# Kernel tuning notes

Measured on AMD Instinct MI355X. Metric: run time of the kernel, lower is better.

The kernel has to match this reference:

```python
import jax, jax.numpy as jnp
import numpy as np

N_HEADS = 16


def setup_inputs() -> dict:
    key = jax.random.key(0)
    k1, k2, k3 = jax.random.split(key, 3)
    B, T, D = 2, 2048, 1024
    x = jax.random.normal(k1, (B, T, D), dtype=jnp.float32)
    w_qkv = jax.random.normal(k2, (3 * D, D), dtype=jnp.float32) * 0.02
    w_proj = jax.random.normal(k3, (D, D), dtype=jnp.float32) * (0.02 / np.sqrt(24.0))
    return {"x": x, "w_qkv": w_qkv, "w_proj": w_proj}


def reference(x, w_qkv, w_proj):
    B, T, D = x.shape
    H = N_HEADS
    dh = D // H
    # qkv linear (no bias): x @ w_qkv.T -> [B, T, 3D]
    qkv = jnp.einsum('btd,ed->bte', x, w_qkv)
    q, k, v = jnp.split(qkv, 3, axis=-1)
    q = q.reshape(B, T, H, dh)
    k = k.reshape(B, T, H, dh)
    v = v.reshape(B, T, H, dh)
    # attention with materialized scores [B, H, T, S]
    scores = jnp.einsum('bthd,bshd->bhts', q, k) / jnp.sqrt(jnp.asarray(dh, x.dtype))
    attn = jax.nn.softmax(scores.astype(jnp.float32), axis=-1).astype(x.dtype)
    out = jnp.einsum('bhts,bshd->bthd', attn, v).reshape(B, T, D)
    # output projection (no bias)
    return jnp.einsum('btd,ed->bte', out, w_proj)
```

## Files before the change

### kernel.cpp

```cpp
#include <hip/hip_runtime.h>


typedef __attribute__((ext_vector_type(8))) short s8v;
typedef __attribute__((ext_vector_type(8))) unsigned short us8;
typedef __attribute__((ext_vector_type(4))) unsigned short us4;
typedef __attribute__((ext_vector_type(4))) float f4v;
typedef __attribute__((ext_vector_type(16))) float f16v;
typedef __attribute__((ext_vector_type(4))) unsigned u4v;

__device__ __forceinline__ unsigned short f2b(float f) {
    unsigned u = __builtin_bit_cast(unsigned, f);
    u += 0x7FFFu + ((u >> 16) & 1u);
    return (unsigned short)(u >> 16);
}
__device__ __forceinline__ unsigned packtrunc(float a, float b, unsigned sel) {
    unsigned r;
    asm("v_perm_b32 %0, %1, %2, %3"
        : "=v"(r)
        : "v"(__builtin_bit_cast(unsigned, b)), "v"(__builtin_bit_cast(unsigned, a)), "s"(sel));
    return r;
}

#if __has_builtin(__builtin_amdgcn_exp2f)
#define EXP2F(x) __builtin_amdgcn_exp2f(x)
#else
#define EXP2F(x) exp2f(x)
#endif

#define QSCALE 0.18033688011112042f

__global__ __launch_bounds__(256) void cvt_all(const float* __restrict__ x,
                                               const float* __restrict__ wq,
                                               const float* __restrict__ wp,
                                               unsigned short* __restrict__ xb,
                                               unsigned short* __restrict__ wqb,
                                               unsigned short* __restrict__ wpb) {
    const int nx = 4096 * 1024 / 4, nq = 3072 * 1024 / 4;
    int i = blockIdx.x * 256 + threadIdx.x;
    const float* s;
    unsigned short* d;
    int j;
    if (i < nx)           { s = x;  d = xb;  j = i; }
    else if (i < nx + nq) { s = wq; d = wqb; j = i - nx; }
    else                  { s = wp; d = wpb; j = i - nx - nq; }
    float4 v = ((const float4*)s)[j];
    ushort4 o;
    o.x = f2b(v.x); o.y = f2b(v.y); o.z = f2b(v.z); o.w = f2b(v.w);
    ((ushort4*)d)[j] = o;
}

#define GLD_LDS16(g, l)                                                                        \
    __builtin_amdgcn_global_load_lds((const __attribute__((address_space(1))) unsigned*)(g),   \
                                     (__attribute__((address_space(3))) unsigned*)(l), 16, 0, 0)

__global__ __launch_bounds__(256) void gemm_qkv(const unsigned short* __restrict__ A,
                                                const unsigned short* __restrict__ B,
                                                unsigned short* __restrict__ qkvb) {
    __shared__ unsigned short As[128][64];
    __shared__ unsigned short Bs[128][64];
    const int tid = threadIdx.x;
    const int l = tid & 63, w = tid >> 6;
    const int quad = l >> 4, ln = l & 15;
    const int m0 = blockIdx.y * 128, n0 = blockIdx.x * 128;
    const int wm = (w >> 1) * 64, wn = (w & 1) * 64;

    const f4v fz = {0.f, 0.f, 0.f, 0.f};
    f4v acc[4][4];
#pragma unroll
    for (int i = 0; i < 4; ++i)
#pragma unroll
        for (int j = 0; j < 4; ++j) acc[i][j] = fz;

    const int srow = tid >> 3, sc8 = tid & 7;
    const int gcol = ((sc8 ^ (srow & 7)) << 3);
    const int koff0 = ((quad ^ (ln & 7)) << 3);
    const int koff1 = (((4 + quad) ^ (ln & 7)) << 3);

    for (int k0 = 0; k0 < 1024; k0 += 64) {
#pragma unroll
        for (int b = 0; b < 4; ++b) {
            GLD_LDS16(A + (size_t)(m0 + srow + 32 * b) * 1024 + k0 + gcol, &As[srow + 32 * b][sc8 * 8]);
            GLD_LDS16(B + (size_t)(n0 + srow + 32 * b) * 1024 + k0 + gcol, &Bs[srow + 32 * b][sc8 * 8]);
        }
        __syncthreads();
#pragma unroll
        for (int ks = 0; ks < 2; ++ks) {
            const int ko = ks ? koff1 : koff0;
            s8v af[4], bf[4];
#pragma unroll
            for (int mt = 0; mt < 4; ++mt) af[mt] = *(const s8v*)&As[wm + mt * 16 + ln][ko];
#pragma unroll
            for (int nt = 0; nt < 4; ++nt) bf[nt] = *(const s8v*)&Bs[wn + nt * 16 + ln][ko];
#pragma unroll
            for (int mt = 0; mt < 4; ++mt)
#pragma unroll
                for (int nt = 0; nt < 4; ++nt)
                    acc[mt][nt] = __builtin_amdgcn_mfma_f32_16x16x32_bf16(af[mt], bf[nt], acc[mt][nt], 0, 0, 0);
        }
        __syncthreads();
    }

#pragma unroll
    for (int mt = 0; mt < 4; ++mt)
#pragma unroll
        for (int nt = 0; nt < 4; ++nt) {
            const int col = n0 + wn + nt * 16 + ln;
            const int row = m0 + wm + mt * 16 + quad * 4;
            const float sc = (col < 1024) ? QSCALE : 1.0f;
#pragma unroll
            for (int r = 0; r < 4; ++r)
                qkvb[(size_t)(row + r) * 3072 + col] = f2b(acc[mt][nt][r] * sc);
        }
}

__global__ __launch_bounds__(256) void gemm_proj(const unsigned short* __restrict__ A,
                                                 const unsigned short* __restrict__ B,
                                                 float* __restrict__ C) {
    __shared__ unsigned short As[128][64];
    __shared__ unsigned short Bs[64][64];
    const int tid = threadIdx.x;
    const int l = tid & 63, w = tid >> 6;
    const int quad = l >> 4, ln = l & 15;
    const int m0 = blockIdx.y * 128, n0 = blockIdx.x * 64;
    const int wm = w * 32;

    const f4v fz = {0.f, 0.f, 0.f, 0.f};
    f4v acc[2][4];
#pragma unroll
    for (int i = 0; i < 2; ++i)
#pragma unroll
        for (int j = 0; j < 4; ++j) acc[i][j] = fz;

    const int srow = tid >> 3, sc8 = tid & 7;
    const int gcol = ((sc8 ^ (srow & 7)) << 3);
    const int koff0 = ((quad ^ (ln & 7)) << 3);
    const int koff1 = (((4 + quad) ^ (ln & 7)) << 3);

    for (int k0 = 0; k0 < 1024; k0 += 64) {
#pragma unroll
        for (int b = 0; b < 4; ++b)
            GLD_LDS16(A + (size_t)(m0 + srow + 32 * b) * 1024 + k0 + gcol, &As[srow + 32 * b][sc8 * 8]);
#pragma unroll
        for (int b = 0; b < 2; ++b)
            GLD_LDS16(B + (size_t)(n0 + srow + 32 * b) * 1024 + k0 + gcol, &Bs[srow + 32 * b][sc8 * 8]);
        __syncthreads();
#pragma unroll
        for (int ks = 0; ks < 2; ++ks) {
            const int ko = ks ? koff1 : koff0;
            s8v af[2], bf[4];
#pragma unroll
            for (int mt = 0; mt < 2; ++mt) af[mt] = *(const s8v*)&As[wm + mt * 16 + ln][ko];
#pragma unroll
            for (int nt = 0; nt < 4; ++nt) bf[nt] = *(const s8v*)&Bs[nt * 16 + ln][ko];
#pragma unroll
            for (int mt = 0; mt < 2; ++mt)
#pragma unroll
                for (int nt = 0; nt < 4; ++nt)
                    acc[mt][nt] = __builtin_amdgcn_mfma_f32_16x16x32_bf16(af[mt], bf[nt], acc[mt][nt], 0, 0, 0);
        }
        __syncthreads();
    }

#pragma unroll
    for (int mt = 0; mt < 2; ++mt)
#pragma unroll
        for (int nt = 0; nt < 4; ++nt) {
            const int row = m0 + wm + mt * 16 + quad * 4;
            const int col = n0 + nt * 16 + ln;
#pragma unroll
            for (int r = 0; r < 4; ++r) C[(size_t)(row + r) * 1024 + col] = acc[mt][nt][r];
        }
}

__global__ __launch_bounds__(256, 4) void attn_split(const unsigned short* __restrict__ qkvb,
                                                     float* __restrict__ opart,
                                                     float* __restrict__ lpart) {
    __shared__ unsigned short Ks[2][64][76];
    __shared__ unsigned short Vt[2][64][76];

    const int tid = threadIdx.x;
    const int l = tid & 63, w = tid >> 6;
    const int m31 = l & 31, h2 = l >> 5;
    const int qw = w * 32;
    const int t0 = blockIdx.x * 128;
    const int hh = blockIdx.y;
    const int bb = blockIdx.z >> 1, sp = blockIdx.z & 1;
    const size_t rowbase = (size_t)bb * 2048;
    const int sbase = sp * 1024;
    const unsigned sel = 0x07060302u;

#pragma unroll
    for (int it = 0; it < 4; ++it) {
        const int idx = tid + it * 256;
        const int qr = idx >> 3, qc = (idx & 7) * 8;
        unsigned short* dst = (qr < 64) ? &Ks[0][qr][qc] : &Ks[1][qr - 64][qc];
        *(us8*)dst = *(const us8*)(qkvb + (rowbase + t0 + qr) * 3072 + hh * 64 + qc);
    }
    __syncthreads();
    s8v qf[4];
    {
        const int qrow = qw + m31;
#pragma unroll
        for (int k4 = 0; k4 < 4; ++k4)
            qf[k4] = (qrow < 64) ? *(const s8v*)&Ks[0][qrow][k4 * 16 + h2 * 8]
                                 : *(const s8v*)&Ks[1][qrow - 64][k4 * 16 + h2 * 8];
    }
    __syncthreads();

    const int r0 = tid >> 3, c0 = (tid & 7) * 8;
    const int va = tid >> 4, vc = tid & 15;

    f16v zz;
#pragma unroll
    for (int i = 0; i < 16; ++i) zz[i] = 0.f;
    f16v oacc[2];
    oacc[0] = zz; oacc[1] = zz;
    float lsum = 0.f;

    us8 kreg0 = *(const us8*)(qkvb + (rowbase + sbase + r0) * 3072 + 1024 + hh * 64 + c0);
    us8 kreg1 = *(const us8*)(qkvb + (rowbase + sbase + r0 + 32) * 3072 + 1024 + hh * 64 + c0);
    us4 vreg[4];
#pragma unroll
    for (int j = 0; j < 4; ++j)
        vreg[j] = *(const us4*)(qkvb + (rowbase + sbase + 4 * va + j) * 3072 + 2048 + hh * 64 + 4 * vc);
    *(us8*)&Ks[0][r0][c0] = kreg0;
    *(us8*)&Ks[0][r0 + 32][c0] = kreg1;
#pragma unroll
    for (int dd = 0; dd < 4; ++dd) {
        unsigned lo = (unsigned)vreg[0][dd] | ((unsigned)vreg[1][dd] << 16);
        unsigned hi = (unsigned)vreg[2][dd] | ((unsigned)vreg[3][dd] << 16);
        uint2 pk2; pk2.x = lo; pk2.y = hi;
        *(uint2*)&Vt[0][4 * vc + dd][4 * va] = pk2;
    }

    for (int i = 0; i < 16; ++i) {
        const int cur = i & 1;
        __syncthreads();

        if (i + 1 < 16) {
            const size_t sn = rowbase + sbase + (i + 1) * 64;
            kreg0 = *(const us8*)(qkvb + (sn + r0) * 3072 + 1024 + hh * 64 + c0);
            kreg1 = *(const us8*)(qkvb + (sn + r0 + 32) * 3072 + 1024 + hh * 64 + c0);
#pragma unroll
            for (int j = 0; j < 4; ++j)
                vreg[j] = *(const us4*)(qkvb + (sn + 4 * va + j) * 3072 + 2048 + hh * 64 + 4 * vc);
        }

#pragma unroll
        for (int st = 0; st < 2; ++st) {
            f16v sacc = zz;
            __builtin_amdgcn_s_setprio(1);
#pragma unroll
            for (int k4 = 0; k4 < 4; ++k4) {
                s8v kf = *(const s8v*)&Ks[cur][st * 32 + m31][k4 * 16 + h2 * 8];
                sacc = __builtin_amdgcn_mfma_f32_32x32x16_bf16(kf, qf[k4], sacc, 0, 0, 0);
            }
            __builtin_amdgcn_s_setprio(0);
            unsigned wv[4][2];
#pragma unroll
            for (int g = 0; g < 4; ++g) {
                float p0 = EXP2F(sacc[g * 4 + 0]);
                float p1 = EXP2F(sacc[g * 4 + 1]);
                float p2 = EXP2F(sacc[g * 4 + 2]);
                float p3 = EXP2F(sacc[g * 4 + 3]);
                lsum += (p0 + p1) + (p2 + p3);
                wv[g][0] = packtrunc(p0, p1, sel);
                wv[g][1] = packtrunc(p2, p3, sel);
            }
            __builtin_amdgcn_s_setprio(1);
#pragma unroll
            for (int e = 0; e < 2; ++e) {
                auto ra = __builtin_amdgcn_permlane32_swap(wv[2 * e][0], wv[2 * e + 1][0], false, false);
                auto rb = __builtin_amdgcn_permlane32_swap(wv[2 * e][1], wv[2 * e + 1][1], false, false);
                u4v t;
                t[0] = ra[0]; t[1] = rb[0];
                t[2] = ra[1]; t[3] = rb[1];
                s8v pf = __builtin_bit_cast(s8v, t);
                const int k2 = 2 * st + e;
#pragma unroll
                for (int nt = 0; nt < 2; ++nt) {
                    s8v vfr = *(const s8v*)&Vt[cur][nt * 32 + m31][k2 * 16 + h2 * 8];
                    oacc[nt] = __builtin_amdgcn_mfma_f32_32x32x16_bf16(pf, vfr, oacc[nt], 0, 0, 0);
                }
            }
            __builtin_amdgcn_s_setprio(0);
        }

        if (i + 1 < 16) {
            *(us8*)&Ks[1 - cur][r0][c0] = kreg0;
            *(us8*)&Ks[1 - cur][r0 + 32][c0] = kreg1;
#pragma unroll
            for (int dd = 0; dd < 4; ++dd) {
                unsigned lo = (unsigned)vreg[0][dd] | ((unsigned)vreg[1][dd] << 16);
                unsigned hi = (unsigned)vreg[2][dd] | ((unsigned)vreg[3][dd] << 16);
                uint2 pk2; pk2.x = lo; pk2.y = hi;
                *(uint2*)&Vt[1 - cur][4 * vc + dd][4 * va] = pk2;
            }
        }
    }

    lsum += __shfl_xor(lsum, 32, 64);
    if (h2 == 0)
        lpart[((size_t)sp * 4096 + rowbase + t0 + qw + m31) * 16 + hh] = lsum;

    float* op = opart + (size_t)sp * 4096 * 1024;
#pragma unroll
    for (int nt = 0; nt < 2; ++nt)
#pragma unroll
        for (int g = 0; g < 4; ++g)
#pragma unroll
            for (int r = 0; r < 4; ++r) {
                const int qrow = 8 * g + 4 * h2 + r;
                op[(rowbase + t0 + qw + qrow) * 1024 + hh * 64 + nt * 32 + m31] = oacc[nt][g * 4 + r];
            }
}

__global__ __launch_bounds__(256) void attn_combine(const float* __restrict__ opart,
                                                    const float* __restrict__ lpart,
                                                    unsigned short* __restrict__ attnb) {
    const int idx = blockIdx.x * 256 + threadIdx.x;
    const int r = idx >> 8, c4 = (idx & 255) << 2, h = c4 >> 6;
    const size_t fi = (size_t)r * 256 + (c4 >> 2);
    float4 o0 = ((const float4*)opart)[fi];
    float4 o1 = ((const float4*)(opart + (size_t)4096 * 1024))[fi];
    float ls = lpart[(size_t)r * 16 + h] + lpart[((size_t)4096 + r) * 16 + h];
    float s = 1.001955f / ls;
    ushort4 o;
    o.x = f2b((o0.x + o1.x) * s);
    o.y = f2b((o0.y + o1.y) * s);
    o.z = f2b((o0.z + o1.z) * s);
    o.w = f2b((o0.w + o1.w) * s);
    ((ushort4*)attnb)[fi] = o;
}

__global__ __launch_bounds__(256) void attn_mfma(const unsigned short* __restrict__ qkvb,
                                                 unsigned short* __restrict__ attnb) {
    __shared__ unsigned short Ks[2][64][76];
    __shared__ unsigned short Vt[2][64][76];
    __shared__ float lred[128];

    const int tid = threadIdx.x;
    const int l = tid & 63, w = tid >> 6;
    const int m31 = l & 31, h2 = l >> 5;
    const int qw = w * 32;
    const int t0 = blockIdx.x * 128;
    const int hh = blockIdx.y, bb = blockIdx.z;
    const size_t rowbase = (size_t)bb * 2048;
    const unsigned sel = 0x07060302u;

#pragma unroll
    for (int it = 0; it < 4; ++it) {
        const int idx = tid + it * 256;
        const int qr = idx >> 3, qc = (idx & 7) * 8;
        unsigned short* dst = (qr < 64) ? &Ks[0][qr][qc] : &Ks[1][qr - 64][qc];
        *(us8*)dst = *(const us8*)(qkvb + (rowbase + t0 + qr) * 3072 + hh * 64 + qc);
    }
    __syncthreads();
    s8v qf[4];
    {
        const int qrow = qw + m31;
#pragma unroll
        for (int k4 = 0; k4 < 4; ++k4)
            qf[k4] = (qrow < 64) ? *(const s8v*)&Ks[0][qrow][k4 * 16 + h2 * 8]
                                 : *(const s8v*)&Ks[1][qrow - 64][k4 * 16 + h2 * 8];
    }
    __syncthreads();

    const int r0 = tid >> 3, c0 = (tid & 7) * 8;
    const int va = tid >> 4, vc = tid & 15;

    f16v zz;
#pragma unroll
    for (int i = 0; i < 16; ++i) zz[i] = 0.f;
    f16v oacc[2];
    oacc[0] = zz; oacc[1] = zz;
    float lsum = 0.f;

    us8 kreg0 = *(const us8*)(qkvb + (rowbase + r0) * 3072 + 1024 + hh * 64 + c0);
    us8 kreg1 = *(const us8*)(qkvb + (rowbase + r0 + 32) * 3072 + 1024 + hh * 64 + c0);
    us4 vreg[4];
#pragma unroll
    for (int j = 0; j < 4; ++j)
        vreg[j] = *(const us4*)(qkvb + (rowbase + 4 * va + j) * 3072 + 2048 + hh * 64 + 4 * vc);
    *(us8*)&Ks[0][r0][c0] = kreg0;
    *(us8*)&Ks[0][r0 + 32][c0] = kreg1;
#pragma unroll
    for (int dd = 0; dd < 4; ++dd) {
        unsigned lo = (unsigned)vreg[0][dd] | ((unsigned)vreg[1][dd] << 16);
        unsigned hi = (unsigned)vreg[2][dd] | ((unsigned)vreg[3][dd] << 16);
        uint2 pk2; pk2.x = lo; pk2.y = hi;
        *(uint2*)&Vt[0][4 * vc + dd][4 * va] = pk2;
    }

    for (int i = 0; i < 32; ++i) {
        const int cur = i & 1;
        __syncthreads();

        if (i + 1 < 32) {
            const int sn = (i + 1) * 64;
            kreg0 = *(const us8*)(qkvb + (rowbase + sn + r0) * 3072 + 1024 + hh * 64 + c0);
            kreg1 = *(const us8*)(qkvb + (rowbase + sn + r0 + 32) * 3072 + 1024 + hh * 64 + c0);
#pragma unroll
            for (int j = 0; j < 4; ++j)
                vreg[j] = *(const us4*)(qkvb + (rowbase + sn + 4 * va + j) * 3072 + 2048 + hh * 64 + 4 * vc);
        }

        f16v sacc[2];
        sacc[0] = zz; sacc[1] = zz;
#pragma unroll
        for (int k4 = 0; k4 < 4; ++k4) {
#pragma unroll
            for (int st = 0; st < 2; ++st) {
                s8v kf = *(const s8v*)&Ks[cur][st * 32 + m31][k4 * 16 + h2 * 8];
                sacc[st] = __builtin_amdgcn_mfma_f32_32x32x16_bf16(kf, qf[k4], sacc[st], 0, 0, 0);
            }
        }

        unsigned wv[2][4][2];
#pragma unroll
        for (int st = 0; st < 2; ++st)
#pragma unroll
            for (int g = 0; g < 4; ++g) {
                float p0 = EXP2F(sacc[st][g * 4 + 0]);
                float p1 = EXP2F(sacc[st][g * 4 + 1]);
                float p2 = EXP2F(sacc[st][g * 4 + 2]);
                float p3 = EXP2F(sacc[st][g * 4 + 3]);
                lsum += (p0 + p1) + (p2 + p3);
                wv[st][g][0] = packtrunc(p0, p1, sel);
                wv[st][g][1] = packtrunc(p2, p3, sel);
            }

        s8v pf[4];
#pragma unroll
        for (int st = 0; st < 2; ++st)
#pragma unroll
            for (int e = 0; e < 2; ++e) {
                auto ra = __builtin_amdgcn_permlane32_swap(wv[st][2 * e][0], wv[st][2 * e + 1][0], false, false);
                auto rb = __builtin_amdgcn_permlane32_swap(wv[st][2 * e][1], wv[st][2 * e + 1][1], false, false);
                u4v t;
                t[0] = ra[0]; t[1] = rb[0];
                t[2] = ra[1]; t[3] = rb[1];
                pf[2 * st + e] = __builtin_bit_cast(s8v, t);
            }

#pragma unroll
        for (int k2 = 0; k2 < 4; ++k2) {
#pragma unroll
            for (int nt = 0; nt < 2; ++nt) {
                s8v vfr = *(const s8v*)&Vt[cur][nt * 32 + m31][k2 * 16 + h2 * 8];
                oacc[nt] = __builtin_amdgcn_mfma_f32_32x32x16_bf16(pf[k2], vfr, oacc[nt], 0, 0, 0);
            }
        }

        if (i + 1 < 32) {
            *(us8*)&Ks[1 - cur][r0][c0] = kreg0;
            *(us8*)&Ks[1 - cur][r0 + 32][c0] = kreg1;
#pragma unroll
            for (int dd = 0; dd < 4; ++dd) {
                unsigned lo = (unsigned)vreg[0][dd] | ((unsigned)vreg[1][dd] << 16);
                unsigned hi = (unsigned)vreg[2][dd] | ((unsigned)vreg[3][dd] << 16);
                uint2 pk2; pk2.x = lo; pk2.y = hi;
                *(uint2*)&Vt[1 - cur][4 * vc + dd][4 * va] = pk2;
            }
        }
    }

    lsum += __shfl_xor(lsum, 32, 64);
    lred[qw + m31] = lsum;
    float inv[16];
#pragma unroll
    for (int g = 0; g < 4; ++g)
#pragma unroll
        for (int r = 0; r < 4; ++r)
            inv[g * 4 + r] = 1.001955f / lred[qw + 8 * g + 4 * h2 + r];

#pragma unroll
    for (int nt = 0; nt < 2; ++nt)
#pragma unroll
        for (int g = 0; g < 4; ++g)
#pragma unroll
            for (int r = 0; r < 4; ++r) {
                const int qrow = 8 * g + 4 * h2 + r;
                float o = oacc[nt][g * 4 + r] * inv[g * 4 + r];
                attnb[(rowbase + t0 + qw + qrow) * 1024 + hh * 64 + nt * 32 + m31] = f2b(o);
            }
}

extern "C" void kernel_launch(void* const* d_in, const int* in_sizes, int n_in,
                              void* d_out, int out_size, void* d_ws, size_t ws_size,
                              hipStream_t stream) {
    const float* x      = (const float*)d_in[0];
    const float* w_qkv  = (const float*)d_in[1];
    const float* w_proj = (const float*)d_in[2];
    float* out = (float*)d_out;

    char* p = (char*)d_ws;
    unsigned short* xb    = (unsigned short*)p;  p += (size_t)4096 * 1024 * 2;
    unsigned short* wqb   = (unsigned short*)p;  p += (size_t)3072 * 1024 * 2;
    unsigned short* wpb   = (unsigned short*)p;  p += (size_t)1024 * 1024 * 2;
    unsigned short* qkvb  = (unsigned short*)p;  p += (size_t)4096 * 3072 * 2;
    unsigned short* attnb = (unsigned short*)p;  p += (size_t)4096 * 1024 * 2;
    float* opart = (float*)p;  p += (size_t)2 * 4096 * 1024 * 4;
    float* lpart = (float*)p;  p += (size_t)2 * 4096 * 16 * 4;
    const size_t need = (size_t)(p - (char*)d_ws);

    cvt_all<<<8192, 256, 0, stream>>>(x, w_qkv, w_proj, xb, wqb, wpb);

    gemm_qkv<<<dim3(3072 / 128, 4096 / 128), 256, 0, stream>>>(xb, wqb, qkvb);

    if (ws_size >= need) {
        attn_split<<<dim3(2048 / 128, 16, 4), 256, 0, stream>>>(qkvb, opart, lpart);
        attn_combine<<<4096, 256, 0, stream>>>(opart, lpart, attnb);
    } else {
        attn_mfma<<<dim3(2048 / 128, 16, 2), 256, 0, stream>>>(qkvb, attnb);
    }

    gemm_proj<<<dim3(1024 / 64, 4096 / 128), 256, 0, stream>>>(attnb, wpb, out);
}
```

Measured before the change: 194.8 us.

## Fuse split-attention combine into output projection GEMM A-tile loads

Removes the separate attn_combine kernel and instead has the projection GEMM read both fp32 attention partials and their row sums, normalise, convert to bf16 and store directly into the LDS A tile. This removes one launch and a bf16 intermediate round trip. The cost is that each column block now re-reads fp32 partials with synchronous loads, which greatly increases A-side traffic. Separately, the QKV GEMM gets a min-blocks launch bound and hoisted load pointers.

```diff
diff --git a/kernel.cpp b/kernel.cpp
--- a/kernel.cpp
+++ b/kernel.cpp
@@ -53,9 +53,9 @@
     __builtin_amdgcn_global_load_lds((const __attribute__((address_space(1))) unsigned*)(g),   \
                                      (__attribute__((address_space(3))) unsigned*)(l), 16, 0, 0)
 
-__global__ __launch_bounds__(256) void gemm_qkv(const unsigned short* __restrict__ A,
-                                                const unsigned short* __restrict__ B,
-                                                unsigned short* __restrict__ qkvb) {
+__global__ __launch_bounds__(256, 4) void gemm_qkv(const unsigned short* __restrict__ A,
+                                                   const unsigned short* __restrict__ B,
+                                                   unsigned short* __restrict__ qkvb) {
     __shared__ unsigned short As[128][64];
     __shared__ unsigned short Bs[128][64];
     const int tid = threadIdx.x;
@@ -76,11 +76,14 @@
     const int koff0 = ((quad ^ (ln & 7)) << 3);
     const int koff1 = (((4 + quad) ^ (ln & 7)) << 3);
 
+    const unsigned short* pa = A + (size_t)(m0 + srow) * 1024 + gcol;
+    const unsigned short* pb = B + (size_t)(n0 + srow) * 1024 + gcol;
+
     for (int k0 = 0; k0 < 1024; k0 += 64) {
 #pragma unroll
         for (int b = 0; b < 4; ++b) {
-            GLD_LDS16(A + (size_t)(m0 + srow + 32 * b) * 1024 + k0 + gcol, &As[srow + 32 * b][sc8 * 8]);
-            GLD_LDS16(B + (size_t)(n0 + srow + 32 * b) * 1024 + k0 + gcol, &Bs[srow + 32 * b][sc8 * 8]);
+            GLD_LDS16(pa + (size_t)32 * b * 1024 + k0, &As[srow + 32 * b][sc8 * 8]);
+            GLD_LDS16(pb + (size_t)32 * b * 1024 + k0, &Bs[srow + 32 * b][sc8 * 8]);
         }
         __syncthreads();
 #pragma unroll
@@ -110,6 +113,82 @@
 #pragma unroll
             for (int r = 0; r < 4; ++r)
                 qkvb[(size_t)(row + r) * 3072 + col] = f2b(acc[mt][nt][r] * sc);
+        }
+}
+
+__global__ __launch_bounds__(256) void gemm_proj_fused(const float* __restrict__ opart,
+                                                       const float* __restrict__ lpart,
+                                                       const unsigned short* __restrict__ Bw,
+                                                       float* __restrict__ C) {
+    __shared__ unsigned short As[128][64];
+    __shared__ unsigned short Bs[64][64];
+    const int tid = threadIdx.x;
+    const int l = tid & 63, w = tid >> 6;
+    const int quad = l >> 4, ln = l & 15;
+    const int m0 = blockIdx.y * 128, n0 = blockIdx.x * 64;
+    const int wm = w * 32;
+
+    const f4v fz = {0.f, 0.f, 0.f, 0.f};
+    f4v acc[2][4];
+#pragma unroll
+    for (int i = 0; i < 2; ++i)
+#pragma unroll
+        for (int j = 0; j < 4; ++j) acc[i][j] = fz;
+
+    const int srow = tid >> 3, sc8 = tid & 7;
+    const int gcol = ((sc8 ^ (srow & 7)) << 3);
+    const int koff0 = ((quad ^ (ln & 7)) << 3);
+    const int koff1 = (((4 + quad) ^ (ln & 7)) << 3);
+
+    for (int k0 = 0; k0 < 1024; k0 += 64) {
+        const int h = k0 >> 6;
+#pragma unroll
+        for (int b = 0; b < 4; ++b) {
+            const int row = m0 + srow + 32 * b;
+            const float* p0 = opart + (size_t)row * 1024 + k0 + gcol;
+            const float* p1 = p0 + (size_t)4096 * 1024;
+            float4 a0 = *(const float4*)p0;
+            float4 a1 = *(const float4*)(p0 + 4);
+            float4 c0 = *(const float4*)p1;
+            float4 c1 = *(const float4*)(p1 + 4);
+            float ls = lpart[(size_t)row * 16 + h] + lpart[((size_t)4096 + row) * 16 + h];
+            float inv = 1.001955f / ls;
+            uint4 pw;
+            pw.x = (unsigned)f2b((a0.x + c0.x) * inv) | ((unsigned)f2b((a0.y + c0.y) * inv) << 16);
+            pw.y = (unsigned)f2b((a0.z + c0.z) * inv) | ((unsigned)f2b((a0.w + c0.w) * inv) << 16);
+            pw.z = (unsigned)f2b((a1.x + c1.x) * inv) | ((unsigned)f2b((a1.y + c1.y) * inv) << 16);
+            pw.w = (unsigned)f2b((a1.z + c1.z) * inv) | ((unsigned)f2b((a1.w + c1.w) * inv) << 16);
+            *(uint4*)&As[srow + 32 * b][sc8 * 8] = pw;
+        }
+#pragma unroll
+        for (int b = 0; b < 2; ++b)
+            GLD_LDS16(Bw + (size_t)(n0 + srow + 32 * b) * 1024 + k0 + gcol, &Bs[srow + 32 * b][sc8 * 8]);
+        __syncthreads();
+#pragma unroll
+        for (int ks = 0; ks < 2; ++ks) {
+            const int ko = ks ? koff1 : koff0;
+            s8v af[2], bf[4];
+#pragma unroll
+            for (int mt = 0; mt < 2; ++mt) af[mt] = *(const s8v*)&As[wm + mt * 16 + ln][ko];
+#pragma unroll
+            for (int nt = 0; nt < 4; ++nt) bf[nt] = *(const s8v*)&Bs[nt * 16 + ln][ko];
+#pragma unroll
+            for (int mt = 0; mt < 2; ++mt)
+#pragma unroll
+                for (int nt = 0; nt < 4; ++nt)
+                    acc[mt][nt] = __builtin_amdgcn_mfma_f32_16x16x32_bf16(af[mt], bf[nt], acc[mt][nt], 0, 0, 0);
+        }
+        __syncthreads();
+    }
+
+#pragma unroll
+    for (int mt = 0; mt < 2; ++mt)
+#pragma unroll
+        for (int nt = 0; nt < 4; ++nt) {
+            const int row = m0 + wm + mt * 16 + quad * 4;
+            const int col = n0 + nt * 16 + ln;
+#pragma unroll
+            for (int r = 0; r < 4; ++r) C[(size_t)(row + r) * 1024 + col] = acc[mt][nt][r];
         }
 }
 
@@ -315,24 +394,6 @@
             }
 }
 
-__global__ __launch_bounds__(256) void attn_combine(const float* __restrict__ opart,
-                                                    const float* __restrict__ lpart,
-                                                    unsigned short* __restrict__ attnb) {
-    const int idx = blockIdx.x * 256 + threadIdx.x;
-    const int r = idx >> 8, c4 = (idx & 255) << 2, h = c4 >> 6;
-    const size_t fi = (size_t)r * 256 + (c4 >> 2);
-    float4 o0 = ((const float4*)opart)[fi];
-    float4 o1 = ((const float4*)(opart + (size_t)4096 * 1024))[fi];
-    float ls = lpart[(size_t)r * 16 + h] + lpart[((size_t)4096 + r) * 16 + h];
-    float s = 1.001955f / ls;
-    ushort4 o;
-    o.x = f2b((o0.x + o1.x) * s);
-    o.y = f2b((o0.y + o1.y) * s);
-    o.z = f2b((o0.z + o1.z) * s);
-    o.w = f2b((o0.w + o1.w) * s);
-    ((ushort4*)attnb)[fi] = o;
-}
-
 __global__ __launch_bounds__(256) void attn_mfma(const unsigned short* __restrict__ qkvb,
                                                  unsigned short* __restrict__ attnb) {
     __shared__ unsigned short Ks[2][64][76];
@@ -510,10 +571,9 @@
 
     if (ws_size >= need) {
         attn_split<<<dim3(2048 / 128, 16, 4), 256, 0, stream>>>(qkvb, opart, lpart);
-        attn_combine<<<4096, 256, 0, stream>>>(opart, lpart, attnb);
+        gemm_proj_fused<<<dim3(1024 / 64, 4096 / 128), 256, 0, stream>>>(opart, lpart, wpb, out);
     } else {
         attn_mfma<<<dim3(2048 / 128, 16, 2), 256, 0, stream>>>(qkvb, attnb);
-    }
-
-    gemm_proj<<<dim3(1024 / 64, 4096 / 128), 256, 0, stream>>>(attnb, wpb, out);
-}
+        gemm_proj<<<dim3(1024 / 64, 4096 / 128), 256, 0, stream>>>(attnb, wpb, out);
+    }
+}
```

Measured after the change: 213.6 us. 9.6% more time.
